# Optimization experiments

Hardware: AMD Instinct MI355X
Metric: run time of the kernel (lower is better)

## Reference

```python
import jax, jax.numpy as jnp
import numpy as np

D_MODEL = 1024
N_HEADS = 16
D_HEAD = D_MODEL // N_HEADS
D_FF = 4096
EPS = 1e-5
NEG = -1e10


def setup_inputs() -> dict:
    key = jax.random.key(0)
    ks = jax.random.split(key, 16)
    s = 0.02
    x = jax.random.normal(ks[0], (4, 1024, D_MODEL), dtype=jnp.float32)
    mask = jnp.ones((4, 1, 1, 1024), dtype=jnp.int32)
    return {
        "x": x,
        "mask": mask,
        "Wq": jax.random.normal(ks[1], (D_MODEL, D_MODEL), jnp.float32) * s,
        "Wk": jax.random.normal(ks[2], (D_MODEL, D_MODEL), jnp.float32) * s,
        "Wv": jax.random.normal(ks[3], (D_MODEL, D_MODEL), jnp.float32) * s,
        "Wp": jax.random.normal(ks[4], (D_MODEL, D_MODEL), jnp.float32) * s,
        "bp": jnp.zeros((D_MODEL,), jnp.float32),
        "W1": jax.random.normal(ks[5], (D_MODEL, D_FF), jnp.float32) * s,
        "b1": jnp.zeros((D_FF,), jnp.float32),
        "W2": jax.random.normal(ks[6], (D_FF, D_MODEL), jnp.float32) * s,
        "b2": jnp.zeros((D_MODEL,), jnp.float32),
        "g1": jnp.ones((D_MODEL,), jnp.float32),
        "be1": jnp.zeros((D_MODEL,), jnp.float32),
        "g2": jnp.ones((D_MODEL,), jnp.float32),
        "be2": jnp.zeros((D_MODEL,), jnp.float32),
    }


def _layer_norm(x, g, b):
    mu = jnp.mean(x, axis=-1, keepdims=True)
    var = jnp.mean(jnp.square(x - mu), axis=-1, keepdims=True)
    return (x - mu) * jax.lax.rsqrt(var + EPS) * g + b


def _mha(x, mask, Wq, Wk, Wv, Wp, bp):
    B, L, _ = x.shape
    q = (x @ Wq).reshape(B, L, N_HEADS, D_HEAD).transpose(0, 2, 1, 3)  # (B,H,L,dh)
    k = (x @ Wk).reshape(B, L, N_HEADS, D_HEAD).transpose(0, 2, 1, 3)
    v = (x @ Wv).reshape(B, L, N_HEADS, D_HEAD).transpose(0, 2, 1, 3)
    scores = jnp.einsum('bhqd,bhkd->bhqk', q, k) / jnp.sqrt(jnp.float32(D_HEAD))
    scores = jnp.where(mask == 0, NEG, scores)
    attn = jax.nn.softmax(scores, axis=-1)
    heads = jnp.einsum('bhqk,bhkd->bhqd', attn, v)  # (B,H,L,dh)
    heads = heads.transpose(0, 2, 1, 3).reshape(B, L, D_MODEL)
    return heads @ Wp + bp


def reference(x, mask, Wq, Wk, Wv, Wp, bp, W1, b1, W2, b2, g1, be1, g2, be2):
    # Post-norm residual sublayers (dropout inactive at inference)
    attn_out = _mha(x, mask, Wq, Wk, Wv, Wp, bp)
    h = _layer_norm(x + attn_out, g1, be1)
    ff = jax.nn.relu(h @ W1 + b1) @ W2 + b2
    out = _layer_norm(h + ff, g2, be2)
    return out
```

## Files before the change

### kernel.cpp

```cpp
#include <hip/hip_runtime.h>
#include <hip/hip_bf16.h>

typedef __attribute__((ext_vector_type(8))) short short8;
typedef __attribute__((ext_vector_type(4))) short short4v;
typedef __attribute__((ext_vector_type(4))) float float4v;

static __device__ __forceinline__ float b2f(short s) {
    return __builtin_bit_cast(float, ((unsigned)(unsigned short)s) << 16);
}
static __device__ __forceinline__ short f2b(float f) {
    unsigned x = __builtin_bit_cast(unsigned, f);
    unsigned r = (x + 0x7fffu + ((x >> 16) & 1u)) >> 16;
    return (short)r;
}
static __device__ __forceinline__ void gload_lds16(const short* g, short* l) {
    __builtin_amdgcn_global_load_lds(
        (const __attribute__((address_space(1))) void*)g,
        (__attribute__((address_space(3))) void*)l, 16, 0, 0);
}

static __device__ __forceinline__ void tile_transpose(const float* __restrict__ in,
                                                      short* __restrict__ out,
                                                      int R, int C, int bx, int by,
                                                      float tile[64][65])
{
    const int tx = threadIdx.x;
    const int r0 = by * 64, c0 = bx * 64;
    const int lr = tx >> 4, lc = (tx & 15) * 4;
#pragma unroll
    for (int p = 0; p < 4; p++) {
        const float4v v = *(const float4v*)&in[(size_t)(r0 + lr + p * 16) * C + c0 + lc];
#pragma unroll
        for (int j = 0; j < 4; j++) tile[lr + p * 16][lc + j] = v[j];
    }
    __syncthreads();
    const int oc = tx >> 3, orr = (tx & 7) * 8;
#pragma unroll
    for (int p = 0; p < 2; p++) {
        const int c = oc + p * 32;
        short8 pk;
#pragma unroll
        for (int j = 0; j < 8; j++) pk[j] = f2b(tile[orr + j][c]);
        *(short8*)&out[(size_t)(c0 + c) * R + r0 + orr] = pk;
    }
}

__global__ __launch_bounds__(256) void prep_k(const float* __restrict__ x,
                                              const float* __restrict__ Wq,
                                              const float* __restrict__ Wk,
                                              const float* __restrict__ Wv,
                                              const float* __restrict__ Wp,
                                              const float* __restrict__ W1,
                                              const float* __restrict__ W2,
                                              short* __restrict__ xb,
                                              short* __restrict__ WqkvT,
                                              short* __restrict__ WpT,
                                              short* __restrict__ W1T,
                                              short* __restrict__ W2T)
{
    __shared__ float tile[64][65];
    const int b = blockIdx.x;
    if (b < 4096) {
        const size_t i = ((size_t)b * 256 + threadIdx.x) * 4;
        const float4v v = *(const float4v*)&x[i];
        short4v s;
#pragma unroll
        for (int j = 0; j < 4; j++) s[j] = f2b(v[j]);
        *(short4v*)&xb[i] = s;
    } else if (b < 5120) {
        const int lb = b - 4096;
        const int wsel = lb >> 8, t = lb & 255;
        const float* in = (wsel == 0) ? Wq : (wsel == 1) ? Wk : (wsel == 2) ? Wv : Wp;
        short* out = (wsel < 3) ? (WqkvT + ((size_t)wsel << 20)) : WpT;
        tile_transpose(in, out, 1024, 1024, t & 15, t >> 4, tile);
    } else if (b < 6144) {
        const int lb = b - 5120;
        tile_transpose(W1, W1T, 1024, 4096, lb & 63, lb >> 6, tile);
    } else {
        const int lb = b - 6144;
        tile_transpose(W2, W2T, 4096, 1024, lb & 15, lb >> 4, tile);
    }
}

template<int MODE, int BM, int BN, int KH>
__global__ __launch_bounds__(256) void gemm_bt(const short* __restrict__ X,
                                               const short* __restrict__ Wt,
                                               short* __restrict__ out,
                                               const float* __restrict__ bias,
                                               const short* __restrict__ res,
                                               int M, int N, int K)
{
    constexpr int MI = BM / 32, NI = BN / 32;
    __shared__ short As[KH][BM * 32];
    __shared__ short Bs[KH][BN * 32];
    const int tid = threadIdx.x;
    const int wave = tid >> 6, lane = tid & 63;
    const int quad = lane >> 4, l16 = lane & 15;

    int bx = blockIdx.x, by = blockIdx.y;
    {
        const int nbx = gridDim.x, nby = gridDim.y;
        if ((nby & 7) == 0) {
            const int g = by * nbx + bx;
            const int xcd = g & 7, local = g >> 3, Y = nby >> 3;
            by = xcd * Y + (local % Y);
            bx = local / Y;
        }
    }
    const int m0 = by * BM, n0 = bx * BN;
    const int wm = (wave >> 1) * (BM / 2), wn = (wave & 1) * (BN / 2);

    int kb = 0, ke = K;
    short* op = out;
    if (MODE == 5) {
        kb = blockIdx.z * (K >> 1);
        ke = kb + (K >> 1);
        op = out + (size_t)blockIdx.z * M * N;
    }

    const int srow = tid >> 2, sc8 = (tid & 3) * 8;

    float4v acc[MI][NI] = {};

    for (int k0 = kb; k0 < ke; k0 += KH * 32) {
#pragma unroll
        for (int c = 0; c < BM / 64; c++)
#pragma unroll
            for (int h = 0; h < KH; h++)
                gload_lds16(X + (size_t)(m0 + c * 64 + srow) * K + k0 + h * 32 + sc8,
                            &As[h][(c * 256 + tid) * 8]);
#pragma unroll
        for (int c = 0; c < BN / 64; c++)
#pragma unroll
            for (int h = 0; h < KH; h++)
                gload_lds16(Wt + (size_t)(n0 + c * 64 + srow) * K + k0 + h * 32 + sc8,
                            &Bs[h][(c * 256 + tid) * 8]);
        __syncthreads();
#pragma unroll
        for (int h = 0; h < KH; h++) {
            short8 af[MI], bf[NI];
#pragma unroll
            for (int i = 0; i < MI; i++) af[i] = *(const short8*)&As[h][(wm + i * 16 + l16) * 32 + quad * 8];
#pragma unroll
            for (int i = 0; i < NI; i++) bf[i] = *(const short8*)&Bs[h][(wn + i * 16 + l16) * 32 + quad * 8];
#pragma unroll
            for (int mi = 0; mi < MI; mi++)
#pragma unroll
                for (int ni = 0; ni < NI; ni++)
                    acc[mi][ni] = __builtin_amdgcn_mfma_f32_16x16x32_bf16(af[mi], bf[ni], acc[mi][ni], 0, 0, 0);
        }
        __syncthreads();
    }

#pragma unroll
    for (int mi = 0; mi < MI; mi++) {
#pragma unroll
        for (int ni = 0; ni < NI; ni++) {
            const int gn = n0 + wn + ni * 16 + l16;
            const float bv = (MODE == 2) ? bias[gn] : 0.0f;
#pragma unroll
            for (int r = 0; r < 4; r++) {
                const int gm = m0 + wm + mi * 16 + quad * 4 + r;
                float v = acc[mi][ni][r];
                if (MODE == 4) {
                    const int s = gn >> 10;
                    const int n = gn & 1023;
                    const int hh = n >> 6, d = n & 63;
                    const size_t bh16 = (size_t)((gm >> 10) * 16 + hh) << 16;
                    const size_t base = (size_t)s << 22;
                    if (s == 0)      out[base + bh16 + ((size_t)(gm & 1023) << 6) + d] = f2b(v * 0.125f);
                    else if (s == 1) out[base + bh16 + ((size_t)(gm & 1023) << 6) + d] = f2b(v);
                    else             out[base + bh16 + ((size_t)d << 10) + (gm & 1023)] = f2b(v);
                } else if (MODE == 2) {
                    v += bv;
                    v = fmaxf(v, 0.0f);
                    out[(size_t)gm * N + gn] = f2b(v);
                } else {
                    op[(size_t)gm * N + gn] = f2b(v);
                }
            }
        }
    }
}

__global__ __launch_bounds__(256) void attn_k(const short* __restrict__ Qb,
                                              const short* __restrict__ Kb,
                                              const short* __restrict__ Vt,
                                              const int* __restrict__ mask,
                                              short* __restrict__ heads)
{
    __shared__ short Kl[2][64 * 32];
    __shared__ short Vl[2][64 * 32];
    __shared__ short P[4][16 * 72];
    const int bh = blockIdx.x, qb = blockIdx.y;
    const int b = bh >> 4, h = bh & 15;
    const int tid = threadIdx.x, wave = tid >> 6, lane = tid & 63;
    const int quad = lane >> 4, l16 = lane & 15;
    const int qbase = qb * 64 + wave * 16;
    const short* Qp = Qb + ((size_t)bh << 16) + (size_t)qbase * 64;
    const short* Kp = Kb + ((size_t)bh << 16);
    const short* Vp = Vt + ((size_t)bh << 16);
    const int* mp = mask + (b << 10);

    const short8 bq0 = *(const short8*)&Qp[l16 * 64 + quad * 8];
    const short8 bq1 = *(const short8*)&Qp[l16 * 64 + 32 + quad * 8];

    float rs = 0.0f;
    float4v o[4] = {};
    short* myP = &P[wave][0];

    const int srow = tid >> 2, sc8 = (tid & 3) * 8;

    for (int kc = 0; kc < 1024; kc += 64) {
        gload_lds16(Kp + (size_t)(kc + srow) * 64 + sc8,      &Kl[0][tid * 8]);
        gload_lds16(Kp + (size_t)(kc + srow) * 64 + 32 + sc8, &Kl[1][tid * 8]);
        gload_lds16(Vp + (size_t)srow * 1024 + kc + sc8,      &Vl[0][tid * 8]);
        gload_lds16(Vp + (size_t)srow * 1024 + kc + 32 + sc8, &Vl[1][tid * 8]);
        __syncthreads();

        float4v s[4];
#pragma unroll
        for (int kt = 0; kt < 4; kt++) {
            s[kt] = (float4v){};
            const short8 ka = *(const short8*)&Kl[0][(kt * 16 + l16) * 32 + quad * 8];
            s[kt] = __builtin_amdgcn_mfma_f32_16x16x32_bf16(ka, bq0, s[kt], 0, 0, 0);
            const short8 kb = *(const short8*)&Kl[1][(kt * 16 + l16) * 32 + quad * 8];
            s[kt] = __builtin_amdgcn_mfma_f32_16x16x32_bf16(kb, bq1, s[kt], 0, 0, 0);
        }
#pragma unroll
        for (int kt = 0; kt < 4; kt++) {
            const int4 mv = *(const int4*)&mp[kc + kt * 16 + quad * 4];
            float p0 = mv.x ? __expf(fminf(s[kt][0], 30.f)) : 0.f;
            float p1 = mv.y ? __expf(fminf(s[kt][1], 30.f)) : 0.f;
            float p2 = mv.z ? __expf(fminf(s[kt][2], 30.f)) : 0.f;
            float p3 = mv.w ? __expf(fminf(s[kt][3], 30.f)) : 0.f;
            rs += (p0 + p1) + (p2 + p3);
            short4v w;
            w[0] = f2b(p0); w[1] = f2b(p1); w[2] = f2b(p2); w[3] = f2b(p3);
            *(short4v*)&myP[l16 * 72 + kt * 16 + quad * 4] = w;
        }
        const short8 bp0 = *(const short8*)&myP[l16 * 72 + quad * 8];
        const short8 bp1 = *(const short8*)&myP[l16 * 72 + 32 + quad * 8];
#pragma unroll
        for (int dt = 0; dt < 4; dt++) {
            const short8 va = *(const short8*)&Vl[0][(dt * 16 + l16) * 32 + quad * 8];
            o[dt] = __builtin_amdgcn_mfma_f32_16x16x32_bf16(va, bp0, o[dt], 0, 0, 0);
            const short8 vb = *(const short8*)&Vl[1][(dt * 16 + l16) * 32 + quad * 8];
            o[dt] = __builtin_amdgcn_mfma_f32_16x16x32_bf16(vb, bp1, o[dt], 0, 0, 0);
        }
        __syncthreads();
    }

    rs += __shfl_xor(rs, 16);
    rs += __shfl_xor(rs, 32);
    const float inv = 1.0f / fmaxf(rs, 1e-20f);
    const int gq = qbase + l16;
#pragma unroll
    for (int dt = 0; dt < 4; dt++) {
        short4v w;
#pragma unroll
        for (int r = 0; r < 4; r++) w[r] = f2b(o[dt][r] * inv);
        *(short4v*)&heads[((size_t)(b * 1024 + gq) << 10) + h * 64 + dt * 16 + quad * 4] = w;
    }
}

template<bool F32OUT>
__global__ __launch_bounds__(256) void red_ln_k(const short* __restrict__ p0,
                                                const short* __restrict__ p1,
                                                const float* __restrict__ bias,
                                                const short* __restrict__ res,
                                                const float* __restrict__ g,
                                                const float* __restrict__ be,
                                                short* __restrict__ outb,
                                                float* __restrict__ outf)
{
    __shared__ float red[8];
    const int row = blockIdx.x, tid = threadIdx.x;
    const size_t base = ((size_t)row << 10) + tid * 4;
    const short4v a = *(const short4v*)&p0[base];
    const short4v b = *(const short4v*)&p1[base];
    const short4v c = *(const short4v*)&res[base];
    const float4v bv = *(const float4v*)&bias[tid * 4];
    float v[4];
#pragma unroll
    for (int i = 0; i < 4; i++) v[i] = b2f(a[i]) + b2f(b[i]) + bv[i] + b2f(c[i]);
    float s = v[0] + v[1] + v[2] + v[3];
#pragma unroll
    for (int off = 32; off; off >>= 1) s += __shfl_xor(s, off);
    if ((tid & 63) == 0) red[tid >> 6] = s;
    __syncthreads();
    const float mu = (red[0] + red[1] + red[2] + red[3]) * (1.0f / 1024.0f);
    float vs = 0.f;
#pragma unroll
    for (int i = 0; i < 4; i++) { const float d = v[i] - mu; vs += d * d; }
#pragma unroll
    for (int off = 32; off; off >>= 1) vs += __shfl_xor(vs, off);
    if ((tid & 63) == 0) red[4 + (tid >> 6)] = vs;
    __syncthreads();
    const float rstd = rsqrtf((red[4] + red[5] + red[6] + red[7]) * (1.0f / 1024.0f) + 1e-5f);
    const float4v gv = *(const float4v*)&g[tid * 4];
    const float4v bev = *(const float4v*)&be[tid * 4];
    if (F32OUT) {
        float4v w;
#pragma unroll
        for (int i = 0; i < 4; i++) w[i] = (v[i] - mu) * rstd * gv[i] + bev[i];
        *(float4v*)&outf[base] = w;
    } else {
        short4v w;
#pragma unroll
        for (int i = 0; i < 4; i++) w[i] = f2b((v[i] - mu) * rstd * gv[i] + bev[i]);
        *(short4v*)&outb[base] = w;
    }
}

extern "C" void kernel_launch(void* const* d_in, const int* in_sizes, int n_in,
                              void* d_out, int out_size, void* d_ws, size_t ws_size,
                              hipStream_t stream)
{
    const float* x   = (const float*)d_in[0];
    const int*   mk  = (const int*)d_in[1];
    const float* Wq  = (const float*)d_in[2];
    const float* Wk  = (const float*)d_in[3];
    const float* Wv  = (const float*)d_in[4];
    const float* Wp  = (const float*)d_in[5];
    const float* bp  = (const float*)d_in[6];
    const float* W1  = (const float*)d_in[7];
    const float* b1  = (const float*)d_in[8];
    const float* W2  = (const float*)d_in[9];
    const float* b2  = (const float*)d_in[10];
    const float* g1  = (const float*)d_in[11];
    const float* be1 = (const float*)d_in[12];
    const float* g2  = (const float*)d_in[13];
    const float* be2 = (const float*)d_in[14];
    float* out = (float*)d_out;

    char* ws = (char*)d_ws;
    const size_t MB = (size_t)1 << 20;
    short* xb     = (short*)(ws + 0 * MB);
    short* WqkvT  = (short*)(ws + 8 * MB);
    short* WpT    = (short*)(ws + 14 * MB);
    short* W1T    = (short*)(ws + 16 * MB);
    short* W2T    = (short*)(ws + 24 * MB);
    short* Qb     = (short*)(ws + 32 * MB);
    short* Kb     = (short*)(ws + 40 * MB);
    short* Vt     = (short*)(ws + 48 * MB);
    short* hd     = (short*)(ws + 56 * MB);
    short* partP  = (short*)(ws + 32 * MB);
    short* u      = (short*)(ws + 32 * MB);
    short* partF  = (short*)(ws + 0 * MB);
    short* hbuf   = (short*)(ws + 72 * MB);

    const dim3 blk(256);

    prep_k<<<dim3(7168), blk, 0, stream>>>(x, Wq, Wk, Wv, Wp, W1, W2,
                                           xb, WqkvT, WpT, W1T, W2T);

    gemm_bt<4, 128, 128, 2><<<dim3(24, 32), blk, 0, stream>>>(xb, WqkvT, Qb, nullptr, nullptr, 4096, 3072, 1024);

    attn_k<<<dim3(64, 16), blk, 0, stream>>>(Qb, Kb, Vt, mk, hd);

    gemm_bt<5, 128, 128, 2><<<dim3(8, 32, 2), blk, 0, stream>>>(hd, WpT, partP, nullptr, nullptr, 4096, 1024, 1024);

    red_ln_k<false><<<dim3(4096), blk, 0, stream>>>(partP, partP + (4u << 20), bp, xb, g1, be1, hbuf, nullptr);

    gemm_bt<2, 128, 128, 2><<<dim3(32, 32), blk, 0, stream>>>(hbuf, W1T, u, b1, nullptr, 4096, 4096, 1024);

    gemm_bt<5, 128, 128, 2><<<dim3(8, 32, 2), blk, 0, stream>>>(u, W2T, partF, nullptr, nullptr, 4096, 1024, 4096);

    red_ln_k<true><<<dim3(4096), blk, 0, stream>>>(partF, partF + (4u << 20), b2, hbuf, g2, be2, nullptr, out);
}
```

Measured before the change: 333.2 us.

## Replace GEMMs with 256x256 8-wave double-buffered kernel and 4-way split-K

Replaces the 128x128 four-wave GEMM with a 256x256 tile, 512-thread kernel. It uses 128KB of dynamic LDS, double-buffered global-to-LDS staging with an XOR swizzle, interleaved barriers with setprio around the MFMA bursts, and ping-pong reuse of A/B fragments. Split-K for the projection and FFN2 GEMMs goes from 2 to 4 partitions, and the LayerNorm reduce kernel now sums four partials. The workspace layout is reshuffled so that the fourth partial fits. The goal is more data reuse per tile and better overlap of loads with compute. The risks are fewer blocks on small grids (192–256 tiles) and more partial-sum traffic.

```diff
diff --git a/kernel.cpp b/kernel.cpp
--- a/kernel.cpp
+++ b/kernel.cpp
@@ -82,86 +82,137 @@
     }
 }
 
-template<int MODE, int BM, int BN, int KH>
-__global__ __launch_bounds__(256) void gemm_bt(const short* __restrict__ X,
-                                               const short* __restrict__ Wt,
-                                               short* __restrict__ out,
-                                               const float* __restrict__ bias,
-                                               const short* __restrict__ res,
-                                               int M, int N, int K)
-{
-    constexpr int MI = BM / 32, NI = BN / 32;
-    __shared__ short As[KH][BM * 32];
-    __shared__ short Bs[KH][BN * 32];
+template<int MODE>
+__global__ __launch_bounds__(512, 2) void gemm8(const short* __restrict__ X,
+                                                const short* __restrict__ Wt,
+                                                short* __restrict__ out,
+                                                const float* __restrict__ bias,
+                                                const short* __restrict__ alt,
+                                                int M, int N, int K)
+{
+    extern __shared__ char lds[];
     const int tid = threadIdx.x;
     const int wave = tid >> 6, lane = tid & 63;
     const int quad = lane >> 4, l16 = lane & 15;
+    const int wm = (wave >> 2) * 128, wn = (wave & 3) * 64;
 
     int bx = blockIdx.x, by = blockIdx.y;
     {
         const int nbx = gridDim.x, nby = gridDim.y;
         if ((nby & 7) == 0) {
             const int g = by * nbx + bx;
-            const int xcd = g & 7, local = g >> 3, Y = nby >> 3;
-            by = xcd * Y + (local % Y);
-            bx = local / Y;
-        }
-    }
-    const int m0 = by * BM, n0 = bx * BN;
-    const int wm = (wave >> 1) * (BM / 2), wn = (wave & 1) * (BN / 2);
-
-    int kb = 0, ke = K;
+            const int xcd = g & 7, loc = g >> 3, Y = nby >> 3;
+            by = xcd * Y + (loc % Y);
+            bx = loc / Y;
+        }
+    }
+    const int m0 = by * 256, n0 = bx * 256;
+
+    int nt = K >> 6, kb = 0;
+    if (MODE == 5) { nt /= (int)gridDim.z; kb = blockIdx.z * nt; }
+
+    const int sr = tid >> 2;
+    const int ce = ((((tid & 3) << 4) ^ ((sr & 3) << 4)) >> 1);
+    const int sx = (l16 & 3) << 4;
+
+    auto stage = [&](int t, int isB, int kh) {
+        const short* src = isB ? Wt : X;
+        const int rb = isB ? n0 : m0;
+        const short* g = src + (size_t)(rb + sr) * K + (size_t)(kb + t) * 64 + kh * 32 + ce;
+        short* d = (short*)(lds + (isB ? 65536 : 0) + ((t & 1) << 15) + (kh << 14)) + tid * 8;
+        gload_lds16(g, d);
+        gload_lds16(g + (size_t)128 * K, d + 4096);
+    };
+
+    float4v acc[8][4] = {};
+    short8 af[4], bf[4];
+
+    auto loadA = [&](int t, int kh, int h) {
+#pragma unroll
+        for (int i = 0; i < 4; i++) {
+            const int row = wm + h * 64 + i * 16 + l16;
+            af[i] = *(const short8*)(lds + ((t & 1) << 15) + (kh << 14) + row * 64 + ((quad << 4) ^ sx));
+        }
+    };
+    auto loadB = [&](int t, int kh) {
+#pragma unroll
+        for (int i = 0; i < 4; i++) {
+            const int row = wn + i * 16 + l16;
+            bf[i] = *(const short8*)(lds + 65536 + ((t & 1) << 15) + (kh << 14) + row * 64 + ((quad << 4) ^ sx));
+        }
+    };
+    auto mmac = [&](int h) {
+#pragma unroll
+        for (int mi = 0; mi < 4; mi++)
+#pragma unroll
+            for (int ni = 0; ni < 4; ni++)
+                acc[h * 4 + mi][ni] = __builtin_amdgcn_mfma_f32_16x16x32_bf16(af[mi], bf[ni], acc[h * 4 + mi][ni], 0, 0, 0);
+    };
+
+    stage(0, 0, 0); stage(0, 1, 0); stage(0, 0, 1); stage(0, 1, 1);
+    asm volatile("s_waitcnt vmcnt(4)" ::: "memory");
+    __builtin_amdgcn_s_barrier();
+
+    for (int t = 0; t < nt - 1; ++t) {
+        loadA(t, 0, 0); loadB(t, 0);
+        stage(t + 1, 0, 0);
+        __builtin_amdgcn_s_barrier();
+        asm volatile("s_waitcnt lgkmcnt(0)" ::: "memory");
+        __builtin_amdgcn_sched_barrier(0);
+        __builtin_amdgcn_s_setprio(1); mmac(0); __builtin_amdgcn_s_setprio(0);
+        __builtin_amdgcn_s_barrier();
+        loadA(t, 0, 1);
+        stage(t + 1, 1, 0);
+        __builtin_amdgcn_s_barrier();
+        asm volatile("s_waitcnt lgkmcnt(0)" ::: "memory");
+        __builtin_amdgcn_sched_barrier(0);
+        __builtin_amdgcn_s_setprio(1); mmac(1); __builtin_amdgcn_s_setprio(0);
+        asm volatile("s_waitcnt vmcnt(4)" ::: "memory");
+        __builtin_amdgcn_s_barrier();
+        loadA(t, 1, 1); loadB(t, 1);
+        stage(t + 1, 0, 1);
+        __builtin_amdgcn_s_barrier();
+        asm volatile("s_waitcnt lgkmcnt(0)" ::: "memory");
+        __builtin_amdgcn_sched_barrier(0);
+        __builtin_amdgcn_s_setprio(1); mmac(1); __builtin_amdgcn_s_setprio(0);
+        __builtin_amdgcn_s_barrier();
+        loadA(t, 1, 0);
+        stage(t + 1, 1, 1);
+        __builtin_amdgcn_s_barrier();
+        asm volatile("s_waitcnt lgkmcnt(0)" ::: "memory");
+        __builtin_amdgcn_sched_barrier(0);
+        __builtin_amdgcn_s_setprio(1); mmac(0); __builtin_amdgcn_s_setprio(0);
+        asm volatile("s_waitcnt vmcnt(4)" ::: "memory");
+        __builtin_amdgcn_s_barrier();
+    }
+    {
+        const int t = nt - 1;
+        loadA(t, 0, 0); loadB(t, 0);
+        mmac(0);
+        loadA(t, 0, 1);
+        mmac(1);
+        asm volatile("s_waitcnt vmcnt(0)" ::: "memory");
+        __builtin_amdgcn_s_barrier();
+        loadA(t, 1, 1); loadB(t, 1);
+        mmac(1);
+        loadA(t, 1, 0);
+        mmac(0);
+    }
+
     short* op = out;
-    if (MODE == 5) {
-        kb = blockIdx.z * (K >> 1);
-        ke = kb + (K >> 1);
-        op = out + (size_t)blockIdx.z * M * N;
-    }
-
-    const int srow = tid >> 2, sc8 = (tid & 3) * 8;
-
-    float4v acc[MI][NI] = {};
-
-    for (int k0 = kb; k0 < ke; k0 += KH * 32) {
-#pragma unroll
-        for (int c = 0; c < BM / 64; c++)
-#pragma unroll
-            for (int h = 0; h < KH; h++)
-                gload_lds16(X + (size_t)(m0 + c * 64 + srow) * K + k0 + h * 32 + sc8,
-                            &As[h][(c * 256 + tid) * 8]);
-#pragma unroll
-        for (int c = 0; c < BN / 64; c++)
-#pragma unroll
-            for (int h = 0; h < KH; h++)
-                gload_lds16(Wt + (size_t)(n0 + c * 64 + srow) * K + k0 + h * 32 + sc8,
-                            &Bs[h][(c * 256 + tid) * 8]);
-        __syncthreads();
-#pragma unroll
-        for (int h = 0; h < KH; h++) {
-            short8 af[MI], bf[NI];
-#pragma unroll
-            for (int i = 0; i < MI; i++) af[i] = *(const short8*)&As[h][(wm + i * 16 + l16) * 32 + quad * 8];
-#pragma unroll
-            for (int i = 0; i < NI; i++) bf[i] = *(const short8*)&Bs[h][(wn + i * 16 + l16) * 32 + quad * 8];
-#pragma unroll
-            for (int mi = 0; mi < MI; mi++)
-#pragma unroll
-                for (int ni = 0; ni < NI; ni++)
-                    acc[mi][ni] = __builtin_amdgcn_mfma_f32_16x16x32_bf16(af[mi], bf[ni], acc[mi][ni], 0, 0, 0);
-        }
-        __syncthreads();
-    }
-
-#pragma unroll
-    for (int mi = 0; mi < MI; mi++) {
-#pragma unroll
-        for (int ni = 0; ni < NI; ni++) {
-            const int gn = n0 + wn + ni * 16 + l16;
+    if (MODE == 5) op = (blockIdx.z == 3 && alt) ? const_cast<short*>(alt)
+                                                 : out + (size_t)blockIdx.z * M * N;
+
+#pragma unroll
+    for (int mf = 0; mf < 8; mf++) {
+#pragma unroll
+        for (int nf = 0; nf < 4; nf++) {
+            const int gn = n0 + wn + nf * 16 + l16;
             const float bv = (MODE == 2) ? bias[gn] : 0.0f;
 #pragma unroll
-            for (int r = 0; r < 4; r++) {
-                const int gm = m0 + wm + mi * 16 + quad * 4 + r;
-                float v = acc[mi][ni][r];
+            for (int rr = 0; rr < 4; rr++) {
+                const int gm = m0 + wm + mf * 16 + (quad << 2) + rr;
+                float v = acc[mf][nf][rr];
                 if (MODE == 4) {
                     const int s = gn >> 10;
                     const int n = gn & 1023;
@@ -172,8 +223,7 @@
                     else if (s == 1) out[base + bh16 + ((size_t)(gm & 1023) << 6) + d] = f2b(v);
                     else             out[base + bh16 + ((size_t)d << 10) + (gm & 1023)] = f2b(v);
                 } else if (MODE == 2) {
-                    v += bv;
-                    v = fmaxf(v, 0.0f);
+                    v = fmaxf(v + bv, 0.0f);
                     out[(size_t)gm * N + gn] = f2b(v);
                 } else {
                     op[(size_t)gm * N + gn] = f2b(v);
@@ -267,6 +317,8 @@
 template<bool F32OUT>
 __global__ __launch_bounds__(256) void red_ln_k(const short* __restrict__ p0,
                                                 const short* __restrict__ p1,
+                                                const short* __restrict__ p2,
+                                                const short* __restrict__ p3,
                                                 const float* __restrict__ bias,
                                                 const short* __restrict__ res,
                                                 const float* __restrict__ g,
@@ -279,11 +331,14 @@
     const size_t base = ((size_t)row << 10) + tid * 4;
     const short4v a = *(const short4v*)&p0[base];
     const short4v b = *(const short4v*)&p1[base];
-    const short4v c = *(const short4v*)&res[base];
+    const short4v c = *(const short4v*)&p2[base];
+    const short4v d = *(const short4v*)&p3[base];
+    const short4v e = *(const short4v*)&res[base];
     const float4v bv = *(const float4v*)&bias[tid * 4];
     float v[4];
 #pragma unroll
-    for (int i = 0; i < 4; i++) v[i] = b2f(a[i]) + b2f(b[i]) + bv[i] + b2f(c[i]);
+    for (int i = 0; i < 4; i++)
+        v[i] = (b2f(a[i]) + b2f(b[i])) + (b2f(c[i]) + b2f(d[i])) + bv[i] + b2f(e[i]);
     float s = v[0] + v[1] + v[2] + v[3];
 #pragma unroll
     for (int off = 32; off; off >>= 1) s += __shfl_xor(s, off);
@@ -292,7 +347,7 @@
     const float mu = (red[0] + red[1] + red[2] + red[3]) * (1.0f / 1024.0f);
     float vs = 0.f;
 #pragma unroll
-    for (int i = 0; i < 4; i++) { const float d = v[i] - mu; vs += d * d; }
+    for (int i = 0; i < 4; i++) { const float dd = v[i] - mu; vs += dd * dd; }
 #pragma unroll
     for (int off = 32; off; off >>= 1) vs += __shfl_xor(vs, off);
     if ((tid & 63) == 0) red[4 + (tid >> 6)] = vs;
@@ -340,32 +395,40 @@
     short* WqkvT  = (short*)(ws + 8 * MB);
     short* WpT    = (short*)(ws + 14 * MB);
     short* W1T    = (short*)(ws + 16 * MB);
-    short* W2T    = (short*)(ws + 24 * MB);
+    short* partP  = (short*)(ws + 24 * MB);
+    short* u      = (short*)(ws + 24 * MB);
     short* Qb     = (short*)(ws + 32 * MB);
-    short* Kb     = (short*)(ws + 40 * MB);
-    short* Vt     = (short*)(ws + 48 * MB);
     short* hd     = (short*)(ws + 56 * MB);
-    short* partP  = (short*)(ws + 32 * MB);
-    short* u      = (short*)(ws + 32 * MB);
+    short* hbuf   = (short*)(ws + 64 * MB);
+    short* W2T    = (short*)(ws + 72 * MB);
     short* partF  = (short*)(ws + 0 * MB);
-    short* hbuf   = (short*)(ws + 72 * MB);
-
-    const dim3 blk(256);
+    short* partF3 = (short*)(ws + 56 * MB);
+
+    hipFuncSetAttribute(reinterpret_cast<const void*>(gemm8<4>),
+                        hipFuncAttributeMaxDynamicSharedMemorySize, 131072);
+    hipFuncSetAttribute(reinterpret_cast<const void*>(gemm8<2>),
+                        hipFuncAttributeMaxDynamicSharedMemorySize, 131072);
+    hipFuncSetAttribute(reinterpret_cast<const void*>(gemm8<5>),
+                        hipFuncAttributeMaxDynamicSharedMemorySize, 131072);
+
+    const dim3 blk(256), blk8(512);
 
     prep_k<<<dim3(7168), blk, 0, stream>>>(x, Wq, Wk, Wv, Wp, W1, W2,
                                            xb, WqkvT, WpT, W1T, W2T);
 
-    gemm_bt<4, 128, 128, 2><<<dim3(24, 32), blk, 0, stream>>>(xb, WqkvT, Qb, nullptr, nullptr, 4096, 3072, 1024);
-
-    attn_k<<<dim3(64, 16), blk, 0, stream>>>(Qb, Kb, Vt, mk, hd);
-
-    gemm_bt<5, 128, 128, 2><<<dim3(8, 32, 2), blk, 0, stream>>>(hd, WpT, partP, nullptr, nullptr, 4096, 1024, 1024);
-
-    red_ln_k<false><<<dim3(4096), blk, 0, stream>>>(partP, partP + (4u << 20), bp, xb, g1, be1, hbuf, nullptr);
-
-    gemm_bt<2, 128, 128, 2><<<dim3(32, 32), blk, 0, stream>>>(hbuf, W1T, u, b1, nullptr, 4096, 4096, 1024);
-
-    gemm_bt<5, 128, 128, 2><<<dim3(8, 32, 2), blk, 0, stream>>>(u, W2T, partF, nullptr, nullptr, 4096, 1024, 4096);
-
-    red_ln_k<true><<<dim3(4096), blk, 0, stream>>>(partF, partF + (4u << 20), b2, hbuf, g2, be2, nullptr, out);
-}
+    gemm8<4><<<dim3(12, 16), blk8, 131072, stream>>>(xb, WqkvT, Qb, nullptr, nullptr, 4096, 3072, 1024);
+
+    attn_k<<<dim3(64, 16), blk, 0, stream>>>(Qb, Qb + (4u << 20), Qb + (8u << 20), mk, hd);
+
+    gemm8<5><<<dim3(4, 16, 4), blk8, 131072, stream>>>(hd, WpT, partP, nullptr, nullptr, 4096, 1024, 1024);
+
+    red_ln_k<false><<<dim3(4096), blk, 0, stream>>>(partP, partP + (4u << 20), partP + (8u << 20), partP + (12u << 20),
+                                                    bp, xb, g1, be1, hbuf, nullptr);
+
+    gemm8<2><<<dim3(16, 16), blk8, 131072, stream>>>(hbuf, W1T, u, b1, nullptr, 4096, 4096, 1024);
+
+    gemm8<5><<<dim3(4, 16, 4), blk8, 131072, stream>>>(u, W2T, partF, nullptr, partF3, 4096, 1024, 4096);
+
+    red_ln_k<true><<<dim3(4096), blk, 0, stream>>>(partF, partF + (4u << 20), partF + (8u << 20), partF3,
+                                                   b2, hbuf, g2, be2, nullptr, out);
+}
```

Result: slower. 347.3 us (+4.3%).

## Swizzle GEMM LDS tiles and raise split-K from two to four

Applied to the files above, without the earlier changes.

The GEMM staging now XOR-swizzles 16-byte chunks by row when loading into LDS and un-swizzles them on fragment reads. This is meant to cut LDS bank conflicts on the MFMA operand loads. The output-projection and W2 GEMMs now split K four ways instead of two, which doubles the block count for better CU fill; the fourth partial goes to a separate buffer. The reduce/LayerNorm kernel sums four partials, which adds extra memory traffic and workspace in exchange.

```diff
diff --git a/kernel.cpp b/kernel.cpp
--- a/kernel.cpp
+++ b/kernel.cpp
@@ -87,7 +87,7 @@
                                                const short* __restrict__ Wt,
                                                short* __restrict__ out,
                                                const float* __restrict__ bias,
-                                               const short* __restrict__ res,
+                                               const short* __restrict__ alt,
                                                int M, int N, int K)
 {
     constexpr int MI = BM / 32, NI = BN / 32;
@@ -113,12 +113,16 @@
     int kb = 0, ke = K;
     short* op = out;
     if (MODE == 5) {
-        kb = blockIdx.z * (K >> 1);
-        ke = kb + (K >> 1);
-        op = out + (size_t)blockIdx.z * M * N;
-    }
-
-    const int srow = tid >> 2, sc8 = (tid & 3) * 8;
+        const int ks = K / (int)gridDim.z;
+        kb = blockIdx.z * ks;
+        ke = kb + ks;
+        op = (blockIdx.z == 3 && alt) ? const_cast<short*>(alt)
+                                      : out + (size_t)blockIdx.z * M * N;
+    }
+
+    const int srow = tid >> 2;
+    const int scs = (((tid & 3) ^ (srow & 3)) * 8);
+    const int rg = ((l16 & 3)) * 8;
 
     float4v acc[MI][NI] = {};
 
@@ -127,22 +131,24 @@
         for (int c = 0; c < BM / 64; c++)
 #pragma unroll
             for (int h = 0; h < KH; h++)
-                gload_lds16(X + (size_t)(m0 + c * 64 + srow) * K + k0 + h * 32 + sc8,
+                gload_lds16(X + (size_t)(m0 + c * 64 + srow) * K + k0 + h * 32 + scs,
                             &As[h][(c * 256 + tid) * 8]);
 #pragma unroll
         for (int c = 0; c < BN / 64; c++)
 #pragma unroll
             for (int h = 0; h < KH; h++)
-                gload_lds16(Wt + (size_t)(n0 + c * 64 + srow) * K + k0 + h * 32 + sc8,
+                gload_lds16(Wt + (size_t)(n0 + c * 64 + srow) * K + k0 + h * 32 + scs,
                             &Bs[h][(c * 256 + tid) * 8]);
         __syncthreads();
 #pragma unroll
         for (int h = 0; h < KH; h++) {
             short8 af[MI], bf[NI];
 #pragma unroll
-            for (int i = 0; i < MI; i++) af[i] = *(const short8*)&As[h][(wm + i * 16 + l16) * 32 + quad * 8];
-#pragma unroll
-            for (int i = 0; i < NI; i++) bf[i] = *(const short8*)&Bs[h][(wn + i * 16 + l16) * 32 + quad * 8];
+            for (int i = 0; i < MI; i++)
+                af[i] = *(const short8*)&As[h][(wm + i * 16 + l16) * 32 + ((quad * 8) ^ rg)];
+#pragma unroll
+            for (int i = 0; i < NI; i++)
+                bf[i] = *(const short8*)&Bs[h][(wn + i * 16 + l16) * 32 + ((quad * 8) ^ rg)];
 #pragma unroll
             for (int mi = 0; mi < MI; mi++)
 #pragma unroll
@@ -267,6 +273,8 @@
 template<bool F32OUT>
 __global__ __launch_bounds__(256) void red_ln_k(const short* __restrict__ p0,
                                                 const short* __restrict__ p1,
+                                                const short* __restrict__ p2,
+                                                const short* __restrict__ p3,
                                                 const float* __restrict__ bias,
                                                 const short* __restrict__ res,
                                                 const float* __restrict__ g,
@@ -279,11 +287,14 @@
     const size_t base = ((size_t)row << 10) + tid * 4;
     const short4v a = *(const short4v*)&p0[base];
     const short4v b = *(const short4v*)&p1[base];
-    const short4v c = *(const short4v*)&res[base];
+    const short4v c = *(const short4v*)&p2[base];
+    const short4v d = *(const short4v*)&p3[base];
+    const short4v e = *(const short4v*)&res[base];
     const float4v bv = *(const float4v*)&bias[tid * 4];
     float v[4];
 #pragma unroll
-    for (int i = 0; i < 4; i++) v[i] = b2f(a[i]) + b2f(b[i]) + bv[i] + b2f(c[i]);
+    for (int i = 0; i < 4; i++)
+        v[i] = (b2f(a[i]) + b2f(b[i])) + (b2f(c[i]) + b2f(d[i])) + bv[i] + b2f(e[i]);
     float s = v[0] + v[1] + v[2] + v[3];
 #pragma unroll
     for (int off = 32; off; off >>= 1) s += __shfl_xor(s, off);
@@ -292,7 +303,7 @@
     const float mu = (red[0] + red[1] + red[2] + red[3]) * (1.0f / 1024.0f);
     float vs = 0.f;
 #pragma unroll
-    for (int i = 0; i < 4; i++) { const float d = v[i] - mu; vs += d * d; }
+    for (int i = 0; i < 4; i++) { const float dd = v[i] - mu; vs += dd * dd; }
 #pragma unroll
     for (int off = 32; off; off >>= 1) vs += __shfl_xor(vs, off);
     if ((tid & 63) == 0) red[4 + (tid >> 6)] = vs;
@@ -346,8 +357,10 @@
     short* Vt     = (short*)(ws + 48 * MB);
     short* hd     = (short*)(ws + 56 * MB);
     short* partP  = (short*)(ws + 32 * MB);
+    short* partP3 = (short*)(ws + 64 * MB);
     short* u      = (short*)(ws + 32 * MB);
     short* partF  = (short*)(ws + 0 * MB);
+    short* partF3 = (short*)(ws + 64 * MB);
     short* hbuf   = (short*)(ws + 72 * MB);
 
     const dim3 blk(256);
@@ -359,13 +372,15 @@
 
     attn_k<<<dim3(64, 16), blk, 0, stream>>>(Qb, Kb, Vt, mk, hd);
 
-    gemm_bt<5, 128, 128, 2><<<dim3(8, 32, 2), blk, 0, stream>>>(hd, WpT, partP, nullptr, nullptr, 4096, 1024, 1024);
-
-    red_ln_k<false><<<dim3(4096), blk, 0, stream>>>(partP, partP + (4u << 20), bp, xb, g1, be1, hbuf, nullptr);
+    gemm_bt<5, 128, 128, 2><<<dim3(8, 32, 4), blk, 0, stream>>>(hd, WpT, partP, nullptr, partP3, 4096, 1024, 1024);
+
+    red_ln_k<false><<<dim3(4096), blk, 0, stream>>>(partP, partP + (4u << 20), partP + (8u << 20), partP3,
+                                                    bp, xb, g1, be1, hbuf, nullptr);
 
     gemm_bt<2, 128, 128, 2><<<dim3(32, 32), blk, 0, stream>>>(hbuf, W1T, u, b1, nullptr, 4096, 4096, 1024);
 
-    gemm_bt<5, 128, 128, 2><<<dim3(8, 32, 2), blk, 0, stream>>>(u, W2T, partF, nullptr, nullptr, 4096, 1024, 4096);
-
-    red_ln_k<true><<<dim3(4096), blk, 0, stream>>>(partF, partF + (4u << 20), b2, hbuf, g2, be2, nullptr, out);
-}
+    gemm_bt<5, 128, 128, 2><<<dim3(8, 32, 4), blk, 0, stream>>>(u, W2T, partF, nullptr, partF3, 4096, 1024, 4096);
+
+    red_ln_k<true><<<dim3(4096), blk, 0, stream>>>(partF, partF + (4u << 20), partF + (8u << 20), partF3,
+                                                   b2, hbuf, g2, be2, nullptr, out);
+}
```

Result: slower. 347.6 us (+4.3%).
